# Performance work log

Hardware: AMD Instinct MI355X
Metric: run time of the kernel (lower is better)

The kernel has to match this reference:

```python
import jax, jax.numpy as jnp
import numpy as np

N_HEADS = 16
MAX_LEN = 1024


def setup_inputs() -> dict:
    key = jax.random.key(0)
    ks = jax.random.split(key, 6)
    B, T, C = 4, 1024, 1024
    scale = 0.02
    return {
        "x": jax.random.normal(ks[0], (B, T, C), dtype=jnp.float32),
        "qkv_w": jax.random.normal(ks[1], (3 * C, C), dtype=jnp.float32) * scale,
        "qkv_b": jax.random.normal(ks[2], (3 * C,), dtype=jnp.float32) * scale,
        "proj_w": jax.random.normal(ks[3], (C, C), dtype=jnp.float32) * scale,
        "proj_b": jax.random.normal(ks[4], (C,), dtype=jnp.float32) * scale,
        "rel_pos_emb": jax.random.normal(ks[5], (2 * MAX_LEN - 1, C), dtype=jnp.float32) * scale,
    }


def reference(x, qkv_w, qkv_b, proj_w, proj_b, rel_pos_emb):
    B, T, C = x.shape
    H = N_HEADS
    D = C // H
    # QKV projection: (B,T,3C) -> (3,B,H,T,D)
    qkv = (x @ qkv_w.T + qkv_b).reshape(B, T, 3, H, D)
    qkv = jnp.transpose(qkv, (2, 0, 3, 1, 4))
    q, k, v = qkv[0], qkv[1], qkv[2]
    # scores: (B,H,T,T)
    att = jnp.einsum("bhtd,bhsd->bhts", q, k) / np.sqrt(D).astype(np.float32)
    # Relative position bias: gather-then-sum == sum-then-gather over head_dim.
    # Pre-reduce table to (2*max_len-1, H) to avoid materializing (T,T,C).
    table = rel_pos_emb.reshape(2 * MAX_LEN - 1, H, D).sum(axis=-1)  # (2L-1, H)
    pos = jnp.arange(T)
    rel_idx = pos[:, None] - pos[None, :] + (MAX_LEN - 1)  # (T,T)
    bias = jnp.transpose(table[rel_idx], (2, 0, 1))  # (H,T,T)
    att = att + bias[None]
    # causal mask: positions j > i masked to -inf
    causal = pos[None, :] > pos[:, None]  # (T,T) True above diagonal
    att = jnp.where(causal[None, None], -jnp.inf, att)
    att = jax.nn.softmax(att, axis=-1)
    out = jnp.einsum("bhts,bhsd->bhtd", att, v)  # (B,H,T,D)
    out = jnp.transpose(out, (0, 2, 1, 3)).reshape(B, T, C)
    return out @ proj_w.T + proj_b
```

## Files before the change

### kernel.cpp

```cpp
#include <hip/hip_runtime.h>
#include <hip/hip_bf16.h>


typedef __bf16 bf16x8 __attribute__((ext_vector_type(8)));
typedef float f32x4 __attribute__((ext_vector_type(4)));

__device__ __forceinline__ float bf2f(unsigned short u) {
    return __uint_as_float(((unsigned)u) << 16);
}
__device__ __forceinline__ unsigned short f2bf(float f) {
    __hip_bfloat16 h = __float2bfloat16(f);
    return *reinterpret_cast<unsigned short*>(&h);
}

__device__ __forceinline__ void gload16(const unsigned short* g, unsigned short* l) {
    __builtin_amdgcn_global_load_lds(
        (const __attribute__((address_space(1))) unsigned int*)(unsigned long long)(const void*)g,
        (__attribute__((address_space(3))) unsigned int*)(unsigned int)(unsigned long long)(void*)l,
        16, 0, 0);
}

__global__ __launch_bounds__(256) void cvt_f32_bf16(const float* __restrict__ in,
                                                    unsigned short* __restrict__ out, int n) {
    int i = (blockIdx.x * 256 + threadIdx.x) * 4;
    if (i < n) {
        float4 v = *(const float4*)(in + i);
        out[i]     = f2bf(v.x);
        out[i + 1] = f2bf(v.y);
        out[i + 2] = f2bf(v.z);
        out[i + 3] = f2bf(v.w);
    }
}

__global__ __launch_bounds__(256) void table_reduce(const float* __restrict__ rel,
                                                    float* __restrict__ table) {
    const int p = blockIdx.x;
    const int tid = threadIdx.x, lane = tid & 63, wave = tid >> 6;
    const float* r = rel + (size_t)p * 1024;
    float s[4];
#pragma unroll
    for (int k = 0; k < 4; ++k) s[k] = r[tid + 256 * k];
#pragma unroll
    for (int k = 0; k < 4; ++k) {
        float v = s[k];
        for (int o = 32; o; o >>= 1) v += __shfl_xor(v, o, 64);
        if (lane == 0) table[p * 16 + wave + 4 * k] = v;
    }
}

template <int EPI>
__global__ __launch_bounds__(256) void gemm_bt(const unsigned short* __restrict__ A,
                                               const unsigned short* __restrict__ Bm,
                                               const float* __restrict__ bias,
                                               unsigned short* __restrict__ outb,
                                               float* __restrict__ outf,
                                               int M, int N, int K) {
    __shared__ __attribute__((aligned(16))) unsigned short As[128 * 32];
    __shared__ __attribute__((aligned(16))) unsigned short Bs[128 * 32];
    const int bm = blockIdx.x * 128, bn = blockIdx.y * 128;
    const int tid = threadIdx.x, lane = tid & 63, wave = tid >> 6;
    const int wr = wave & 1, wc = wave >> 1;
    const int quad = lane >> 4, lm = lane & 15;

    const int srow = wave * 32 + (lane >> 2);
    const int scol = (lane & 3) * 8;
    const unsigned short* Ap = A + (size_t)(bm + srow) * K + scol;
    const unsigned short* Bp = Bm + (size_t)(bn + srow) * K + scol;
    unsigned short* AsD0 = &As[(wave * 32) * 32];
    unsigned short* AsD1 = &As[(wave * 32 + 16) * 32];
    unsigned short* BsD0 = &Bs[(wave * 32) * 32];
    unsigned short* BsD1 = &Bs[(wave * 32 + 16) * 32];

    f32x4 acc[4][4];
#pragma unroll
    for (int r = 0; r < 4; ++r)
#pragma unroll
        for (int c = 0; c < 4; ++c) acc[r][c] = (f32x4){0.f, 0.f, 0.f, 0.f};

    for (int kk = 0; kk < K; kk += 32) {
        __syncthreads();
        gload16(Ap + kk, AsD0);
        gload16(Ap + (size_t)16 * K + kk, AsD1);
        gload16(Bp + kk, BsD0);
        gload16(Bp + (size_t)16 * K + kk, BsD1);
        __syncthreads();

        bf16x8 af[4], bfr[4];
#pragma unroll
        for (int r = 0; r < 4; ++r)
            af[r] = *(const bf16x8*)(&As[(64 * wr + 16 * r + lm) * 32 + quad * 8]);
#pragma unroll
        for (int c = 0; c < 4; ++c)
            bfr[c] = *(const bf16x8*)(&Bs[(64 * wc + 16 * c + lm) * 32 + quad * 8]);
#pragma unroll
        for (int r = 0; r < 4; ++r)
#pragma unroll
            for (int c = 0; c < 4; ++c)
                acc[r][c] = __builtin_amdgcn_mfma_f32_16x16x32_bf16(af[r], bfr[c], acc[r][c], 0, 0, 0);
    }

#pragma unroll
    for (int r = 0; r < 4; ++r)
#pragma unroll
        for (int c = 0; c < 4; ++c)
#pragma unroll
            for (int i = 0; i < 4; ++i) {
                const int row = bm + 64 * wr + 16 * r + quad * 4 + i;
                const int col = bn + 64 * wc + 16 * c + lm;
                const float v = acc[r][c][i] + bias[col];
                if (EPI == 0) {
                    const int b = row >> 10, t = row & 1023;
                    const int s3 = col >> 10, rem = col & 1023;
                    const int h = rem >> 6, d = rem & 63;
                    const size_t base = (((size_t)s3 * 4 + b) * 16 + h) * 65536;
                    const size_t off = base + (s3 == 2 ? (size_t)d * 1024 + t
                                                       : (size_t)t * 64 + d);
                    outb[off] = f2bf(v);
                } else {
                    outf[(size_t)row * N + col] = v;
                }
            }
}

__global__ __launch_bounds__(256) void attn_mfma(const unsigned short* __restrict__ qkvb,
                                                 const float* __restrict__ table,
                                                 unsigned short* __restrict__ y) {
    const int bh = blockIdx.x, b = bh >> 4, h = bh & 15;
    const int qb = blockIdx.y * 64;
    const int tid = threadIdx.x, lane = tid & 63, wave = tid >> 6;
    const int quad = lane >> 4, lm = lane & 15;

    __shared__ __attribute__((aligned(16))) unsigned short Ks[64][72];
    __shared__ __attribute__((aligned(16))) unsigned short Vs[64][72];
    __shared__ __attribute__((aligned(16))) unsigned short Ps[4][16][72];
    __shared__ float tb[1088];

    const unsigned short* Qg  = qkvb + ((size_t)(b)*16 + h) * 65536;
    const unsigned short* Kg  = qkvb + ((size_t)(4 + b)*16 + h) * 65536;
    const unsigned short* Vtg = qkvb + ((size_t)(8 + b)*16 + h) * 65536;

    const bf16x8 qf0 = *(const bf16x8*)(Qg + (size_t)(qb + wave * 16 + lm) * 64 + quad * 8);
    const bf16x8 qf1 = *(const bf16x8*)(Qg + (size_t)(qb + wave * 16 + lm) * 64 + 32 + quad * 8);

    const int tbn = qb + 127;
    for (int i = tid; i < tbn; i += 256) tb[i] = table[(960 + i) * 16 + h];

    f32x4 oacc[4];
#pragma unroll
    for (int nb = 0; nb < 4; ++nb) oacc[nb] = (f32x4){0.f, 0.f, 0.f, 0.f};
    float mi[4], li[4];
#pragma unroll
    for (int i = 0; i < 4; ++i) { mi[i] = -1e30f; li[i] = 0.f; }

    const int ktiles = qb / 64 + 1;
    for (int kt = 0; kt < ktiles; ++kt) {
        __syncthreads();
        {
            const int r0 = tid >> 3, c0 = (tid & 7) * 8, r1 = r0 + 32;
            *(int4*)&Ks[r0][c0] = *(const int4*)(Kg + (size_t)(kt * 64 + r0) * 64 + c0);
            *(int4*)&Ks[r1][c0] = *(const int4*)(Kg + (size_t)(kt * 64 + r1) * 64 + c0);
            *(int4*)&Vs[r0][c0] = *(const int4*)(Vtg + (size_t)r0 * 1024 + kt * 64 + c0);
            *(int4*)&Vs[r1][c0] = *(const int4*)(Vtg + (size_t)r1 * 1024 + kt * 64 + c0);
        }
        __syncthreads();

        f32x4 s[4];
#pragma unroll
        for (int nb = 0; nb < 4; ++nb) {
            bf16x8 k0 = *(const bf16x8*)(&Ks[nb * 16 + lm][quad * 8]);
            bf16x8 k1 = *(const bf16x8*)(&Ks[nb * 16 + lm][32 + quad * 8]);
            s[nb] = (f32x4){0.f, 0.f, 0.f, 0.f};
            s[nb] = __builtin_amdgcn_mfma_f32_16x16x32_bf16(qf0, k0, s[nb], 0, 0, 0);
            s[nb] = __builtin_amdgcn_mfma_f32_16x16x32_bf16(qf1, k1, s[nb], 0, 0, 0);
        }

        const int qrow0 = qb + wave * 16 + quad * 4;
        const int jbase = kt * 64 + lm;
#pragma unroll
        for (int nb = 0; nb < 4; ++nb)
#pragma unroll
            for (int i = 0; i < 4; ++i) {
                const int q = qrow0 + i, j = jbase + nb * 16;
                const float v = fmaf(s[nb][i], 0.125f, tb[q - j + 63]);
                s[nb][i] = (j <= q) ? v : -1e30f;
            }

        float mnew[4], al[4];
#pragma unroll
        for (int i = 0; i < 4; ++i) {
            float mx = fmaxf(fmaxf(s[0][i], s[1][i]), fmaxf(s[2][i], s[3][i]));
            mx = fmaxf(mx, __shfl_xor(mx, 1, 64));
            mx = fmaxf(mx, __shfl_xor(mx, 2, 64));
            mx = fmaxf(mx, __shfl_xor(mx, 4, 64));
            mx = fmaxf(mx, __shfl_xor(mx, 8, 64));
            mnew[i] = fmaxf(mi[i], mx);
            al[i] = __expf(mi[i] - mnew[i]);
            mi[i] = mnew[i];
        }
#pragma unroll
        for (int nb = 0; nb < 4; ++nb)
#pragma unroll
            for (int i = 0; i < 4; ++i) s[nb][i] = __expf(s[nb][i] - mnew[i]);
#pragma unroll
        for (int i = 0; i < 4; ++i) {
            float sm = (s[0][i] + s[1][i]) + (s[2][i] + s[3][i]);
            sm += __shfl_xor(sm, 1, 64);
            sm += __shfl_xor(sm, 2, 64);
            sm += __shfl_xor(sm, 4, 64);
            sm += __shfl_xor(sm, 8, 64);
            li[i] = li[i] * al[i] + sm;
        }

#pragma unroll
        for (int nb = 0; nb < 4; ++nb)
#pragma unroll
            for (int i = 0; i < 4; ++i)
                Ps[wave][quad * 4 + i][nb * 16 + lm] = f2bf(s[nb][i]);

#pragma unroll
        for (int nb = 0; nb < 4; ++nb)
#pragma unroll
            for (int i = 0; i < 4; ++i) oacc[nb][i] *= al[i];

        const bf16x8 p0 = *(const bf16x8*)(&Ps[wave][lm][quad * 8]);
        const bf16x8 p1 = *(const bf16x8*)(&Ps[wave][lm][32 + quad * 8]);
#pragma unroll
        for (int nb = 0; nb < 4; ++nb) {
            bf16x8 v0 = *(const bf16x8*)(&Vs[nb * 16 + lm][quad * 8]);
            bf16x8 v1 = *(const bf16x8*)(&Vs[nb * 16 + lm][32 + quad * 8]);
            oacc[nb] = __builtin_amdgcn_mfma_f32_16x16x32_bf16(p0, v0, oacc[nb], 0, 0, 0);
            oacc[nb] = __builtin_amdgcn_mfma_f32_16x16x32_bf16(p1, v1, oacc[nb], 0, 0, 0);
        }
    }

    float inv[4];
#pragma unroll
    for (int i = 0; i < 4; ++i) inv[i] = 1.0f / li[i];
#pragma unroll
    for (int nb = 0; nb < 4; ++nb)
#pragma unroll
        for (int i = 0; i < 4; ++i) {
            const int q = qb + wave * 16 + quad * 4 + i;
            const int d = nb * 16 + lm;
            y[((size_t)(b * 1024 + q)) * 1024 + h * 64 + d] = f2bf(oacc[nb][i] * inv[i]);
        }
}

extern "C" void kernel_launch(void* const* d_in, const int* in_sizes, int n_in,
                              void* d_out, int out_size, void* d_ws, size_t ws_size,
                              hipStream_t stream) {
    const float* x      = (const float*)d_in[0];
    const float* qkv_w  = (const float*)d_in[1];
    const float* qkv_b  = (const float*)d_in[2];
    const float* proj_w = (const float*)d_in[3];
    const float* proj_b = (const float*)d_in[4];
    const float* rel    = (const float*)d_in[5];
    float* out = (float*)d_out;

    char* ws = (char*)d_ws;
    unsigned short* xb   = (unsigned short*)(ws);
    unsigned short* wb   = (unsigned short*)(ws + 8388608);
    unsigned short* pwb  = (unsigned short*)(ws + 14680064);
    float* table         = (float*)(ws + 16777216);
    unsigned short* qkvb = (unsigned short*)(ws + 16908288);
    unsigned short* yb   = (unsigned short*)(ws + 42074112);

    cvt_f32_bf16<<<4096, 256, 0, stream>>>(x, xb, 4194304);
    cvt_f32_bf16<<<3072, 256, 0, stream>>>(qkv_w, wb, 3145728);
    cvt_f32_bf16<<<1024, 256, 0, stream>>>(proj_w, pwb, 1048576);
    table_reduce<<<2047, 256, 0, stream>>>(rel, table);
    gemm_bt<0><<<dim3(32, 24), 256, 0, stream>>>(xb, wb, qkv_b, qkvb, nullptr, 4096, 3072, 1024);
    attn_mfma<<<dim3(64, 16), 256, 0, stream>>>(qkvb, table, yb);
    gemm_bt<1><<<dim3(32, 8), 256, 0, stream>>>(yb, pwb, proj_b, nullptr, out, 4096, 1024, 1024);
}
```

Baseline: 226.0 us.

## Register-prefetch GEMM tiles and pad LDS rows to avoid bank conflicts

Replaces the direct global-to-LDS async loads in the bf16 GEMM with register-staged loads. The next K-tile is prefetched into registers while MFMAs run on the current tile. LDS rows are padded from 32 to 40 elements to reduce bank conflicts on the fragment reads. In exchange it uses more registers and adds an extra LDS store pass per iteration.

```diff
diff --git a/kernel.cpp b/kernel.cpp
--- a/kernel.cpp
+++ b/kernel.cpp
@@ -11,13 +11,6 @@
 __device__ __forceinline__ unsigned short f2bf(float f) {
     __hip_bfloat16 h = __float2bfloat16(f);
     return *reinterpret_cast<unsigned short*>(&h);
-}
-
-__device__ __forceinline__ void gload16(const unsigned short* g, unsigned short* l) {
-    __builtin_amdgcn_global_load_lds(
-        (const __attribute__((address_space(1))) unsigned int*)(unsigned long long)(const void*)g,
-        (__attribute__((address_space(3))) unsigned int*)(unsigned int)(unsigned long long)(void*)l,
-        16, 0, 0);
 }
 
 __global__ __launch_bounds__(256) void cvt_f32_bf16(const float* __restrict__ in,
@@ -55,21 +48,19 @@
                                                unsigned short* __restrict__ outb,
                                                float* __restrict__ outf,
                                                int M, int N, int K) {
-    __shared__ __attribute__((aligned(16))) unsigned short As[128 * 32];
-    __shared__ __attribute__((aligned(16))) unsigned short Bs[128 * 32];
+    __shared__ __attribute__((aligned(16))) unsigned short As[128 * 40];
+    __shared__ __attribute__((aligned(16))) unsigned short Bs[128 * 40];
     const int bm = blockIdx.x * 128, bn = blockIdx.y * 128;
     const int tid = threadIdx.x, lane = tid & 63, wave = tid >> 6;
     const int wr = wave & 1, wc = wave >> 1;
     const int quad = lane >> 4, lm = lane & 15;
 
-    const int srow = wave * 32 + (lane >> 2);
-    const int scol = (lane & 3) * 8;
+    const int srow = tid >> 1;
+    const int scol = (tid & 1) * 16;
     const unsigned short* Ap = A + (size_t)(bm + srow) * K + scol;
     const unsigned short* Bp = Bm + (size_t)(bn + srow) * K + scol;
-    unsigned short* AsD0 = &As[(wave * 32) * 32];
-    unsigned short* AsD1 = &As[(wave * 32 + 16) * 32];
-    unsigned short* BsD0 = &Bs[(wave * 32) * 32];
-    unsigned short* BsD1 = &Bs[(wave * 32 + 16) * 32];
+    unsigned short* AsW = &As[srow * 40 + scol];
+    unsigned short* BsW = &Bs[srow * 40 + scol];
 
     f32x4 acc[4][4];
 #pragma unroll
@@ -77,26 +68,38 @@
 #pragma unroll
         for (int c = 0; c < 4; ++c) acc[r][c] = (f32x4){0.f, 0.f, 0.f, 0.f};
 
+    int4 pa0 = *(const int4*)(Ap);
+    int4 pa1 = *(const int4*)(Ap + 8);
+    int4 pb0 = *(const int4*)(Bp);
+    int4 pb1 = *(const int4*)(Bp + 8);
+
     for (int kk = 0; kk < K; kk += 32) {
-        __syncthreads();
-        gload16(Ap + kk, AsD0);
-        gload16(Ap + (size_t)16 * K + kk, AsD1);
-        gload16(Bp + kk, BsD0);
-        gload16(Bp + (size_t)16 * K + kk, BsD1);
-        __syncthreads();
+        *(int4*)(AsW)     = pa0;
+        *(int4*)(AsW + 8) = pa1;
+        *(int4*)(BsW)     = pb0;
+        *(int4*)(BsW + 8) = pb1;
+        __syncthreads();
+
+        if (kk + 32 < K) {
+            pa0 = *(const int4*)(Ap + kk + 32);
+            pa1 = *(const int4*)(Ap + kk + 40);
+            pb0 = *(const int4*)(Bp + kk + 32);
+            pb1 = *(const int4*)(Bp + kk + 40);
+        }
 
         bf16x8 af[4], bfr[4];
 #pragma unroll
         for (int r = 0; r < 4; ++r)
-            af[r] = *(const bf16x8*)(&As[(64 * wr + 16 * r + lm) * 32 + quad * 8]);
+            af[r] = *(const bf16x8*)(&As[(64 * wr + 16 * r + lm) * 40 + quad * 8]);
 #pragma unroll
         for (int c = 0; c < 4; ++c)
-            bfr[c] = *(const bf16x8*)(&Bs[(64 * wc + 16 * c + lm) * 32 + quad * 8]);
+            bfr[c] = *(const bf16x8*)(&Bs[(64 * wc + 16 * c + lm) * 40 + quad * 8]);
 #pragma unroll
         for (int r = 0; r < 4; ++r)
 #pragma unroll
             for (int c = 0; c < 4; ++c)
                 acc[r][c] = __builtin_amdgcn_mfma_f32_16x16x32_bf16(af[r], bfr[c], acc[r][c], 0, 0, 0);
+        __syncthreads();
     }
 
 #pragma unroll
```

New measurement: 219.9 us. -2.7%, faster.
